# Optimization experiments

Measured on AMD Instinct MI355X. Metric: run time of the kernel, lower is better.

The kernel has to match this reference:

```python
import jax, jax.numpy as jnp
import numpy as np

B, N, D = 4, 2048, 1024  # in_features == out_features required by the original code path
SPARSITY = 0.01


def setup_inputs() -> dict:
    key = jax.random.key(0)
    k1, k2, k3 = jax.random.split(key, 3)
    x = jax.random.normal(k1, (B, N, D), dtype=jnp.float32)
    # Reproduce FrequencyLinearLayer.__init__: sparse top-k frequency weights.
    spatial = jax.random.normal(k2, (D, D), dtype=jnp.float32) * 0.02
    freq = jnp.fft.fft(spatial, axis=-1)  # complex64, (out, in) consumed as (D_in, D_out)
    k = int(D * SPARSITY)
    mag = jnp.abs(freq)
    kth = jax.lax.top_k(mag, k)[0][:, -1:]  # k-th largest magnitude per row
    w_sparse = jnp.where(mag >= kth, freq, 0.0 + 0.0j)
    bias = jax.random.normal(k3, (D,), dtype=jnp.float32) * 0.01
    return {
        "x": x,
        "w_freq_real": jnp.real(w_sparse).astype(jnp.float32),
        "w_freq_imag": jnp.imag(w_sparse).astype(jnp.float32),
        "bias": bias,
    }


def reference(x, w_freq_real, w_freq_imag, bias):
    # y = real(IFFT(FFT(x) @ W_freq)) + bias
    # The original materializes a (B,N,D_in,D_out) complex intermediate via
    # unsqueeze*multiply -> sum; that is exactly a complex matmul, expressed here as einsum.
    w = jax.lax.complex(w_freq_real, w_freq_imag)            # (D_in, D_out) complex64
    x_freq = jnp.fft.fft(x, axis=-1)                          # (B, N, D_in) complex64
    y_freq = jnp.einsum('bnd,do->bno', x_freq, w)             # (B, N, D_out)
    y = jnp.real(jnp.fft.ifft(y_freq, axis=-1))               # (B, N, D_out) float32
    return y + bias
```

## Files before the change

### kernel.cpp

```cpp
#include <hip/hip_runtime.h>
#include <hip/hip_bf16.h>
#include <math.h>

#define DD 1024
#define BT 8192
#define TWO_PI 6.28318530717958647692f

typedef float f32x4 __attribute__((ext_vector_type(4)));
typedef short bf16x8 __attribute__((ext_vector_type(8)));
typedef unsigned short u16x8 __attribute__((ext_vector_type(8)));
typedef unsigned short u16x4 __attribute__((ext_vector_type(4)));
typedef const __attribute__((address_space(1))) void g_void;
typedef __attribute__((address_space(3))) void l_void;

__device__ __forceinline__ unsigned short f2bf(float f) {
  unsigned int u = __float_as_uint(f);
  unsigned int r = (u + 0x7FFFu + ((u >> 16) & 1u)) >> 16;
  return (unsigned short)r;
}

__global__ __launch_bounds__(256) void build_G_kernel(
    const float* __restrict__ Wr, const float* __restrict__ Wi,
    float2* __restrict__ Gf) {
  __shared__ float2 tw[DD];
  __shared__ int    oidx[64];
  __shared__ float2 wval[64];
  __shared__ int    sc[256];
  const int k = blockIdx.x, tid = threadIdx.x;

  for (int j = tid; j < DD; j += 256) {
    float s, c;
    sincosf((TWO_PI / DD) * (float)j, &s, &c);
    tw[j] = make_float2(c, s);
  }
  int cnt = 0;
  float2 wl[4];
  int    ol[4];
#pragma unroll
  for (int q = 0; q < 4; q++) {
    int o = tid + q * 256;
    float wr = Wr[(size_t)k * DD + o];
    float wi = Wi[(size_t)k * DD + o];
    if (wr != 0.f || wi != 0.f) { wl[cnt] = make_float2(wr, wi); ol[cnt] = o; cnt++; }
  }
  sc[tid] = cnt;
  __syncthreads();
#pragma unroll
  for (int dstep = 1; dstep < 256; dstep <<= 1) {
    int v = (tid >= dstep) ? sc[tid - dstep] : 0;
    __syncthreads();
    sc[tid] += v;
    __syncthreads();
  }
  int p = sc[tid] - cnt;
  for (int q = 0; q < cnt; q++) { oidx[p + q] = ol[q]; wval[p + q] = wl[q]; }
  __syncthreads();
  const int nnz = sc[255];
  for (int m = tid; m < DD; m += 256) {
    float re = 0.f, im = 0.f;
    for (int j = 0; j < nnz; j++) {
      int    o  = oidx[j];
      float2 w  = wval[j];
      float2 cs = tw[(o * m) & (DD - 1)];
      re += w.x * cs.x - w.y * cs.y;
      im += w.x * cs.y + w.y * cs.x;
    }
    Gf[(size_t)k * DD + m] = make_float2(re, im);
  }
}

__global__ __launch_bounds__(256) void transpose_G_kernel(
    const float2* __restrict__ Gf, unsigned short* __restrict__ Gt) {
  __shared__ float2 tile[64][65];
  const int k0 = blockIdx.x * 64, m0 = blockIdx.y * 64;
  for (int q = threadIdx.x; q < 64 * 64; q += 256) {
    int r = q >> 6, c = q & 63;
    tile[r][c] = Gf[(size_t)(k0 + r) * DD + m0 + c];
  }
  __syncthreads();
  for (int q = threadIdx.x; q < 64 * 64; q += 256) {
    int r = q >> 6, c = q & 63;
    float2 v = tile[c][r];
    Gt[(size_t)(m0 + r) * 2048 + k0 + c]        = f2bf(v.x);
    Gt[(size_t)(m0 + r) * 2048 + 1024 + k0 + c] = f2bf(v.y);
  }
}

__global__ __launch_bounds__(256) void build_M_convert_kernel(
    const unsigned short* __restrict__ Gt,
    float* __restrict__ P,
    const float* __restrict__ X, unsigned short* __restrict__ Xb) {
  __shared__ __align__(16) unsigned short Asm[128 * 32];
  __shared__ __align__(16) unsigned short Bsm[128 * 32];
  const int tid = threadIdx.x;

  if (blockIdx.x >= 256) {
    size_t i = (size_t)(blockIdx.x - 256) * 256 + tid;
    const float4* p = (const float4*)(X + i * 8);
    float4 a = p[0], c = p[1];
    u16x8 v;
    v[0] = f2bf(a.x); v[1] = f2bf(a.y); v[2] = f2bf(a.z); v[3] = f2bf(a.w);
    v[4] = f2bf(c.x); v[5] = f2bf(c.y); v[6] = f2bf(c.z); v[7] = f2bf(c.w);
    *(u16x8*)(Xb + i * 8) = v;
    return;
  }

  const int wave = tid >> 6, lane = tid & 63;
  const int wr = wave >> 1, wc = wave & 1;
  const int col0 = (blockIdx.x & 7) * 128;
  const int row0 = ((blockIdx.x >> 3) & 7) * 128;
  const int bz   = blockIdx.x >> 6;
  const int kBeg = bz * 512;

  f32x4 acc[4][4] = {};

  for (int k0 = kBeg; k0 < kBeg + 512; k0 += 32) {
    __syncthreads();
#pragma unroll
    for (int is = 0; is < 2; is++) {
      int e = is * 256 + tid;
      int r = e >> 2, c = (e & 3) * 8;
      const unsigned short* ga = Gt + (size_t)(row0 + r) * 2048 + k0 + c;
      __builtin_amdgcn_global_load_lds((g_void*)ga,
          (l_void*)(Asm + is * 2048 + wave * 512), 16, 0, 0);
    }
#pragma unroll
    for (int is = 0; is < 2; is++) {
      int e = is * 256 + tid;
      int r = e >> 2, c = (e & 3) * 8;
      int d = col0 + r;
      u16x8 v;
#pragma unroll
      for (int q = 0; q < 8; q++) {
        int K   = k0 + c + q;
        int idx = (K * d) & (DD - 1);
        float s, cc;
        __sincosf((TWO_PI / DD) * (float)idx, &s, &cc);
        v[q] = f2bf((K < DD) ? cc : s);
      }
      *(u16x8*)(Bsm + e * 8) = v;
    }
    __syncthreads();

    bf16x8 af[4], bfr[4];
#pragma unroll
    for (int i = 0; i < 4; i++) {
      int ra = wr * 64 + i * 16 + (lane & 15);
      af[i]  = *(const bf16x8*)&Asm[ra * 32 + (lane >> 4) * 8];
      int rb = wc * 64 + i * 16 + (lane & 15);
      bfr[i] = *(const bf16x8*)&Bsm[rb * 32 + (lane >> 4) * 8];
    }
#pragma unroll
    for (int i = 0; i < 4; i++)
#pragma unroll
      for (int j = 0; j < 4; j++)
        acc[i][j] = __builtin_amdgcn_mfma_f32_16x16x32_bf16(af[i], bfr[j], acc[i][j], 0, 0, 0);
  }

  const int crow0 = row0 + wr * 64;
  const int ccol0 = col0 + wc * 64;
  float* O = P + (size_t)bz * DD * DD;
#pragma unroll
  for (int i = 0; i < 4; i++)
#pragma unroll
    for (int j = 0; j < 4; j++) {
      int cc = ccol0 + j * 16 + (lane & 15);
#pragma unroll
      for (int v = 0; v < 4; v++) {
        int rr = crow0 + i * 16 + (lane >> 4) * 4 + v;
        O[(size_t)rr * DD + cc] = acc[i][j][v];
      }
    }
}

__global__ __launch_bounds__(256) void reduce_M_kernel(
    const float* __restrict__ P, unsigned short* __restrict__ Mb) {
  const size_t NE = (size_t)DD * DD;
  size_t i = ((size_t)blockIdx.x * 256 + threadIdx.x) * 4;
  float4 s = *(const float4*)(P + i);
#pragma unroll
  for (int z = 1; z < 4; z++) {
    float4 p = *(const float4*)(P + z * NE + i);
    s.x += p.x; s.y += p.y; s.z += p.z; s.w += p.w;
  }
  const float inv = 1.0f / (float)DD;
  u16x4 v;
  v[0] = f2bf(s.x * inv); v[1] = f2bf(s.y * inv);
  v[2] = f2bf(s.z * inv); v[3] = f2bf(s.w * inv);
  *(u16x4*)(Mb + i) = v;
}

__global__ __launch_bounds__(256) void gemm_y_kernel(
    const unsigned short* __restrict__ Xb,
    const unsigned short* __restrict__ Mb,
    const float* __restrict__ bias,
    float* __restrict__ Y) {
  __shared__ __align__(16) unsigned short Asm[128 * 32];
  __shared__ __align__(16) unsigned short Bsm[128 * 32];
  const int tid  = threadIdx.x;
  const int wave = tid >> 6, lane = tid & 63;
  const int wr = wave >> 1, wc = wave & 1;

  const int L  = blockIdx.x;
  const int w  = (L & 7) * 64 + (L >> 3);
  const int row0 = (w >> 3) * 128;
  const int col0 = (w & 7) * 128;

  f32x4 acc[4][4] = {};

  for (int k0 = 0; k0 < DD; k0 += 32) {
    __syncthreads();
#pragma unroll
    for (int is = 0; is < 2; is++) {
      int e = is * 256 + tid;
      int r = e >> 2, c = (e & 3) * 8;
      const unsigned short* ga = Xb + (size_t)(row0 + r) * DD + k0 + c;
      const unsigned short* gb = Mb + (size_t)(col0 + r) * DD + k0 + c;
      __builtin_amdgcn_global_load_lds((g_void*)ga,
          (l_void*)(Asm + is * 2048 + wave * 512), 16, 0, 0);
      __builtin_amdgcn_global_load_lds((g_void*)gb,
          (l_void*)(Bsm + is * 2048 + wave * 512), 16, 0, 0);
    }
    __syncthreads();

    bf16x8 af[4], bfr[4];
#pragma unroll
    for (int i = 0; i < 4; i++) {
      int ra = wr * 64 + i * 16 + (lane & 15);
      af[i]  = *(const bf16x8*)&Asm[ra * 32 + (lane >> 4) * 8];
      int rb = wc * 64 + i * 16 + (lane & 15);
      bfr[i] = *(const bf16x8*)&Bsm[rb * 32 + (lane >> 4) * 8];
    }
#pragma unroll
    for (int i = 0; i < 4; i++)
#pragma unroll
      for (int j = 0; j < 4; j++)
        acc[i][j] = __builtin_amdgcn_mfma_f32_16x16x32_bf16(af[i], bfr[j], acc[i][j], 0, 0, 0);
  }

  const int crow0 = row0 + wr * 64;
  const int ccol0 = col0 + wc * 64;
  float bv[4];
#pragma unroll
  for (int j = 0; j < 4; j++)
    bv[j] = bias[ccol0 + j * 16 + (lane & 15)];
#pragma unroll
  for (int i = 0; i < 4; i++)
#pragma unroll
    for (int j = 0; j < 4; j++) {
      int cc = ccol0 + j * 16 + (lane & 15);
#pragma unroll
      for (int v = 0; v < 4; v++) {
        int rr = crow0 + i * 16 + (lane >> 4) * 4 + v;
        Y[(size_t)rr * DD + cc] = acc[i][j][v] + bv[j];
      }
    }
}

extern "C" void kernel_launch(void* const* d_in, const int* in_sizes, int n_in,
                              void* d_out, int out_size, void* d_ws, size_t ws_size,
                              hipStream_t stream) {
  const float* x    = (const float*)d_in[0];
  const float* wrp  = (const float*)d_in[1];
  const float* wip  = (const float*)d_in[2];
  const float* bias = (const float*)d_in[3];
  float*       y    = (float*)d_out;

  char* ws = (char*)d_ws;
  const size_t MB = 1024 * 1024;
  float2*         Gf = (float2*)(ws + 0);
  unsigned short* Gt = (unsigned short*)(ws + 8 * MB);
  unsigned short* Mb = (unsigned short*)(ws + 12 * MB);
  float*          P  = (float*)(ws + 16 * MB);
  unsigned short* Xb = (unsigned short*)(ws + 32 * MB);

  build_G_kernel<<<DD, 256, 0, stream>>>(wrp, wip, Gf);
  transpose_G_kernel<<<dim3(16, 16), 256, 0, stream>>>(Gf, Gt);
  build_M_convert_kernel<<<4352, 256, 0, stream>>>(Gt, P, x, Xb);
  reduce_M_kernel<<<DD, 256, 0, stream>>>(P, Mb);
  gemm_y_kernel<<<512, 256, 0, stream>>>(Xb, Mb, bias, y);
}
```

Measured before the change: 87.70 us.

## Fuse split-K reduction into build_M via last-block atomic counter

```diff
diff --git a/kernel.cpp b/kernel.cpp
--- a/kernel.cpp
+++ b/kernel.cpp
@@ -21,19 +21,21 @@
 
 __global__ __launch_bounds__(256) void build_G_kernel(
     const float* __restrict__ Wr, const float* __restrict__ Wi,
-    float2* __restrict__ Gf) {
+    float2* __restrict__ Gf, int* __restrict__ cnt) {
   __shared__ float2 tw[DD];
   __shared__ int    oidx[64];
   __shared__ float2 wval[64];
   __shared__ int    sc[256];
   const int k = blockIdx.x, tid = threadIdx.x;
 
+  if (k == 0 && tid < 64) cnt[tid] = 0;
+
   for (int j = tid; j < DD; j += 256) {
     float s, c;
     sincosf((TWO_PI / DD) * (float)j, &s, &c);
     tw[j] = make_float2(c, s);
   }
-  int cnt = 0;
+  int cnt_l = 0;
   float2 wl[4];
   int    ol[4];
 #pragma unroll
@@ -41,9 +43,9 @@
     int o = tid + q * 256;
     float wr = Wr[(size_t)k * DD + o];
     float wi = Wi[(size_t)k * DD + o];
-    if (wr != 0.f || wi != 0.f) { wl[cnt] = make_float2(wr, wi); ol[cnt] = o; cnt++; }
-  }
-  sc[tid] = cnt;
+    if (wr != 0.f || wi != 0.f) { wl[cnt_l] = make_float2(wr, wi); ol[cnt_l] = o; cnt_l++; }
+  }
+  sc[tid] = cnt_l;
   __syncthreads();
 #pragma unroll
   for (int dstep = 1; dstep < 256; dstep <<= 1) {
@@ -52,8 +54,8 @@
     sc[tid] += v;
     __syncthreads();
   }
-  int p = sc[tid] - cnt;
-  for (int q = 0; q < cnt; q++) { oidx[p + q] = ol[q]; wval[p + q] = wl[q]; }
+  int p = sc[tid] - cnt_l;
+  for (int q = 0; q < cnt_l; q++) { oidx[p + q] = ol[q]; wval[p + q] = wl[q]; }
   __syncthreads();
   const int nnz = sc[255];
   for (int m = tid; m < DD; m += 256) {
@@ -89,9 +91,11 @@
 __global__ __launch_bounds__(256) void build_M_convert_kernel(
     const unsigned short* __restrict__ Gt,
     float* __restrict__ P,
-    const float* __restrict__ X, unsigned short* __restrict__ Xb) {
+    const float* __restrict__ X, unsigned short* __restrict__ Xb,
+    unsigned short* __restrict__ Mb, int* __restrict__ cnt) {
   __shared__ __align__(16) unsigned short Asm[128 * 32];
   __shared__ __align__(16) unsigned short Bsm[128 * 32];
+  __shared__ int oldv;
   const int tid = threadIdx.x;
 
   if (blockIdx.x >= 256) {
@@ -110,6 +114,7 @@
   const int col0 = (blockIdx.x & 7) * 128;
   const int row0 = ((blockIdx.x >> 3) & 7) * 128;
   const int bz   = blockIdx.x >> 6;
+  const int tileId = blockIdx.x & 63;
   const int kBeg = bz * 512;
 
   f32x4 acc[4][4] = {};
@@ -168,26 +173,35 @@
 #pragma unroll
       for (int v = 0; v < 4; v++) {
         int rr = crow0 + i * 16 + (lane >> 4) * 4 + v;
-        O[(size_t)rr * DD + cc] = acc[i][j][v];
-      }
-    }
-}
-
-__global__ __launch_bounds__(256) void reduce_M_kernel(
-    const float* __restrict__ P, unsigned short* __restrict__ Mb) {
-  const size_t NE = (size_t)DD * DD;
-  size_t i = ((size_t)blockIdx.x * 256 + threadIdx.x) * 4;
-  float4 s = *(const float4*)(P + i);
-#pragma unroll
-  for (int z = 1; z < 4; z++) {
-    float4 p = *(const float4*)(P + z * NE + i);
-    s.x += p.x; s.y += p.y; s.z += p.z; s.w += p.w;
-  }
-  const float inv = 1.0f / (float)DD;
-  u16x4 v;
-  v[0] = f2bf(s.x * inv); v[1] = f2bf(s.y * inv);
-  v[2] = f2bf(s.z * inv); v[3] = f2bf(s.w * inv);
-  *(u16x4*)(Mb + i) = v;
+        __builtin_nontemporal_store(acc[i][j][v], &O[(size_t)rr * DD + cc]);
+      }
+    }
+
+  __threadfence();
+  if (tid == 0) oldv = atomicAdd(&cnt[tileId], 1);
+  __syncthreads();
+  if (oldv == 3) {
+    __threadfence();
+    const size_t NE = (size_t)DD * DD;
+    const float inv = 1.0f / (float)DD;
+#pragma unroll
+    for (int q = 0; q < 16; q++) {
+      int e  = q * 256 + tid;
+      int r  = e >> 5;
+      int c4 = (e & 31) * 4;
+      size_t idx = (size_t)(row0 + r) * DD + col0 + c4;
+      float4 s = *(const float4*)(P + idx);
+#pragma unroll
+      for (int z = 1; z < 4; z++) {
+        float4 p = *(const float4*)(P + z * NE + idx);
+        s.x += p.x; s.y += p.y; s.z += p.z; s.w += p.w;
+      }
+      u16x4 v;
+      v[0] = f2bf(s.x * inv); v[1] = f2bf(s.y * inv);
+      v[2] = f2bf(s.z * inv); v[3] = f2bf(s.w * inv);
+      *(u16x4*)(Mb + idx) = v;
+    }
+  }
 }
 
 __global__ __launch_bounds__(256) void gemm_y_kernel(
@@ -252,7 +266,7 @@
 #pragma unroll
       for (int v = 0; v < 4; v++) {
         int rr = crow0 + i * 16 + (lane >> 4) * 4 + v;
-        Y[(size_t)rr * DD + cc] = acc[i][j][v] + bv[j];
+        __builtin_nontemporal_store(acc[i][j][v] + bv[j], &Y[(size_t)rr * DD + cc]);
       }
     }
 }
@@ -268,15 +282,15 @@
 
   char* ws = (char*)d_ws;
   const size_t MB = 1024 * 1024;
-  float2*         Gf = (float2*)(ws + 0);
-  unsigned short* Gt = (unsigned short*)(ws + 8 * MB);
-  unsigned short* Mb = (unsigned short*)(ws + 12 * MB);
-  float*          P  = (float*)(ws + 16 * MB);
-  unsigned short* Xb = (unsigned short*)(ws + 32 * MB);
-
-  build_G_kernel<<<DD, 256, 0, stream>>>(wrp, wip, Gf);
+  float2*         Gf  = (float2*)(ws + 0);
+  unsigned short* Gt  = (unsigned short*)(ws + 8 * MB);
+  unsigned short* Mb  = (unsigned short*)(ws + 12 * MB);
+  float*          P   = (float*)(ws + 16 * MB);
+  unsigned short* Xb  = (unsigned short*)(ws + 32 * MB);
+  int*            cnt = (int*)(ws + 48 * MB);
+
+  build_G_kernel<<<DD, 256, 0, stream>>>(wrp, wip, Gf, cnt);
   transpose_G_kernel<<<dim3(16, 16), 256, 0, stream>>>(Gf, Gt);
-  build_M_convert_kernel<<<4352, 256, 0, stream>>>(Gt, P, x, Xb);
-  reduce_M_kernel<<<DD, 256, 0, stream>>>(P, Mb);
+  build_M_convert_kernel<<<4352, 256, 0, stream>>>(Gt, P, x, Xb, Mb, cnt);
   gemm_y_kernel<<<512, 256, 0, stream>>>(Xb, Mb, bias, y);
 }
```

Result: slower. 129.3 us (+47.5%).
